# Kernel tuning notes

Measured on AMD Instinct MI355X. Metric: run time of the kernel, lower is better.

## Reference

```python
import jax, jax.numpy as jnp
import numpy as np

B, DIM, HGT, WID = 2, 384, 256, 256
HEADS = 8


def setup_inputs() -> dict:
    key = jax.random.key(0)
    k0, k1, k2, k3 = jax.random.split(key, 4)
    x = jax.random.normal(k0, (B, DIM, HGT, WID), jnp.float32)
    # 1x1 conv weights stored as (out_ch, in_ch); depthwise 3x3 as (out_ch, 1, 3, 3)
    qkv_w = jax.random.normal(k1, (3 * DIM, DIM), jnp.float32) * 0.02
    dw_w = jax.random.normal(k2, (3 * DIM, 1, 3, 3), jnp.float32) * 0.02
    proj_w = jax.random.normal(k3, (DIM, DIM), jnp.float32) * 0.02
    log_temp = jnp.zeros((HEADS, 1, 1), jnp.float32)  # nn.Parameter init zeros
    return {"x": x, "qkv_w": qkv_w, "dw_w": dw_w, "proj_w": proj_w, "log_temp": log_temp}


def _l2norm_lastdim(t):
    # F.normalize(t, dim=-1): t / max(||t||_2, eps), eps=1e-12
    n = jnp.linalg.norm(t, axis=-1, keepdims=True)
    return t / jnp.maximum(n, 1e-12)


def reference(x, qkv_w, dw_w, proj_w, log_temp):
    b, c, h, w = x.shape
    heads = log_temp.shape[0]
    head_dim = c // heads

    # 1x1 conv (pointwise) -> channel GEMM
    qkv = jnp.einsum('bchw,oc->bohw', x, qkv_w)
    # depthwise 3x3, stride 1, pad 1, groups = 3*dim
    qkv = jax.lax.conv_general_dilated(
        qkv, dw_w, window_strides=(1, 1), padding=[(1, 1), (1, 1)],
        dimension_numbers=('NCHW', 'OIHW', 'NCHW'), feature_group_count=3 * c)

    q, k, v = jnp.split(qkv, 3, axis=1)
    rs = lambda t: t.reshape(b, heads, head_dim, h * w)
    q, k, v = rs(q), rs(k), rs(v)

    q = _l2norm_lastdim(q)
    k = _l2norm_lastdim(k)

    # channel-wise attention: (head_dim x head_dim) logits per (b, head)
    attn = jnp.einsum('bhcn,bhdn->bhcd', q, k)
    attn = attn * (jax.nn.softplus(log_temp) + 1e-6)
    attn = jax.nn.softmax(attn, axis=-1)

    out = jnp.einsum('bhcd,bhdn->bhcn', attn, v).reshape(b, c, h, w)
    return jnp.einsum('bchw,oc->bohw', out, proj_w)
```

## Files before the change

kernel.cpp:

```cpp
#include <hip/hip_runtime.h>
#include <cstdint>
#include <cstddef>

#define HW 65536
#define HGT 256
#define WID 256
#define CDIM 384
#define C3 1152
#define HEADS 8
#define HD 48
#define NCHUNK 128
#define CHUNK (HW / NCHUNK)

typedef unsigned short u16;
typedef __attribute__((ext_vector_type(8))) short short8;
typedef __attribute__((ext_vector_type(16))) float f32x16;
typedef __attribute__((ext_vector_type(4))) u16 us4;

__device__ __forceinline__ u16 f2bf_rn(float f) {
  uint32_t u = __float_as_uint(f);
  return (u16)((u + 0x7FFFu + ((u >> 16) & 1u)) >> 16);
}
__device__ __forceinline__ float bf2f(u16 s) {
  return __uint_as_float((uint32_t)s << 16);
}

__device__ __forceinline__ void stage16(const void* g, void* lds_wave_base) {
  __builtin_amdgcn_global_load_lds(
      (const __attribute__((address_space(1))) void*)g,
      (__attribute__((address_space(3))) void*)lds_wave_base, 16, 0, 0);
}

__global__ __launch_bounds__(256)
void mfma_gemm_split(const u16* __restrict__ Ah, const u16* __restrict__ Al,
                     const u16* __restrict__ Bh, const u16* __restrict__ Bl,
                     float* __restrict__ C, int N, int K, int m_tiles) {
  __shared__ u16 sm[4][4096];
  const int t = threadIdx.x;
  const int wid = t >> 6, lane = t & 63;
  const int w = blockIdx.x;
  const int xcd = w & 7;
  const int slot = w >> 3;
  const int npx = (int)(gridDim.x >> 3) / m_tiles;
  const int m0 = (slot % m_tiles) * 128;
  const int n0 = (xcd * npx + slot / m_tiles) * 128;
  const int wm = (wid >> 1) * 64, wn = (wid & 1) * 64;

  f32x16 acc[2][2];
#pragma unroll
  for (int i = 0; i < 2; i++)
#pragma unroll
    for (int j = 0; j < 2; j++)
#pragma unroll
      for (int r = 0; r < 16; r++) acc[i][j][r] = 0.f;

  for (int k0 = 0; k0 < K; k0 += 32) {
#pragma unroll
    for (int u = 0; u < 2; u++) {
      const int s = u * 256 + wid * 64 + lane;
      const int row = s >> 2;
      const int cd = (s & 3) ^ ((row >> 1) & 3);
      const size_t offA = (size_t)(m0 + row) * K + k0 + cd * 8;
      const size_t offB = (size_t)(n0 + row) * K + k0 + cd * 8;
      const int lb = (u * 256 + wid * 64) * 8;
      stage16(Ah + offA, &sm[0][lb]);
      stage16(Al + offA, &sm[1][lb]);
      stage16(Bh + offB, &sm[2][lb]);
      stage16(Bl + offB, &sm[3][lb]);
    }
    __syncthreads();

    short8 ah[2][2], al[2][2], bh[2][2], bl[2][2];
#pragma unroll
    for (int f = 0; f < 2; f++)
#pragma unroll
      for (int ks = 0; ks < 2; ks++) {
        const int ra = wm + f * 32 + (lane & 31);
        const int ca = (ks * 2 + (lane >> 5)) ^ ((ra >> 1) & 3);
        const int oa = ra * 32 + ca * 8;
        ah[f][ks] = *(const short8*)&sm[0][oa];
        al[f][ks] = *(const short8*)&sm[1][oa];
        const int rb = wn + f * 32 + (lane & 31);
        const int cb = (ks * 2 + (lane >> 5)) ^ ((rb >> 1) & 3);
        const int ob = rb * 32 + cb * 8;
        bh[f][ks] = *(const short8*)&sm[2][ob];
        bl[f][ks] = *(const short8*)&sm[3][ob];
      }
#pragma unroll
    for (int ks = 0; ks < 2; ks++)
#pragma unroll
      for (int i = 0; i < 2; i++)
#pragma unroll
        for (int j = 0; j < 2; j++) {
          acc[i][j] = __builtin_amdgcn_mfma_f32_32x32x16_bf16(ah[i][ks], bh[j][ks], acc[i][j], 0, 0, 0);
          acc[i][j] = __builtin_amdgcn_mfma_f32_32x32x16_bf16(ah[i][ks], bl[j][ks], acc[i][j], 0, 0, 0);
          acc[i][j] = __builtin_amdgcn_mfma_f32_32x32x16_bf16(al[i][ks], bh[j][ks], acc[i][j], 0, 0, 0);
        }
    __syncthreads();
  }
  float* Cb = C + (size_t)(m0 + wm) * N + n0 + wn;
#pragma unroll
  for (int i = 0; i < 2; i++)
#pragma unroll
    for (int j = 0; j < 2; j++) {
      const int cc = j * 32 + (lane & 31);
#pragma unroll
      for (int reg = 0; reg < 16; reg++) {
        const int rr = i * 32 + (reg & 3) + 8 * (reg >> 2) + 4 * (lane >> 5);
        Cb[(size_t)rr * N + cc] = acc[i][j][reg];
      }
    }
}

__global__ __launch_bounds__(256)
void transpose_cvt(const float* __restrict__ in, u16* __restrict__ hi,
                   u16* __restrict__ lo) {
  __shared__ float tbuf[64][65];
  const int n0 = blockIdx.x * 64, c0 = blockIdx.y * 64;
  const int tx = threadIdx.x & 63, ty = threadIdx.x >> 6;
#pragma unroll
  for (int c = ty; c < 64; c += 4)
    tbuf[tx][c] = in[(size_t)(c0 + c) * HW + n0 + tx];
  __syncthreads();
  const int cq = (threadIdx.x & 15) << 2;
  const int nb = threadIdx.x >> 4;
#pragma unroll
  for (int p = 0; p < 4; p++) {
    const int n = p * 16 + nb;
    us4 h, l;
#pragma unroll
    for (int i = 0; i < 4; i++) {
      float f = tbuf[n][cq + i];
      u16 hb = f2bf_rn(f);
      h[i] = hb;
      l[i] = f2bf_rn(f - bf2f(hb));
    }
    *(us4*)&hi[(size_t)(n0 + n) * CDIM + c0 + cq] = h;
    *(us4*)&lo[(size_t)(n0 + n) * CDIM + c0 + cq] = l;
  }
}

__global__ __launch_bounds__(256)
void split_cvt(const float* __restrict__ in, u16* __restrict__ hi,
               u16* __restrict__ lo, int n) {
  int i = blockIdx.x * 256 + threadIdx.x;
  if (i < n) {
    float f = in[i];
    u16 hb = f2bf_rn(f);
    hi[i] = hb;
    lo[i] = f2bf_rn(f - bf2f(hb));
  }
}

__global__ __launch_bounds__(256)
void dwconv3x3(const float* __restrict__ in, const float* __restrict__ wgt,
               float* __restrict__ out) {
  const int ch = blockIdx.y;
  const int y0 = blockIdx.x * 4;
  const int t = threadIdx.x;
  __shared__ float rows[6][264];
  const float* inc = in + (size_t)ch * HW;
  float w9[9];
#pragma unroll
  for (int k = 0; k < 9; k++) w9[k] = wgt[ch * 9 + k];
  if (t < 6) {
    rows[t][0] = 0.f;
    rows[t][WID + 1] = 0.f;
  }
  for (int i = t; i < 6 * WID; i += 256) {
    int r = i >> 8;
    int x = i & 255;
    int y = y0 - 1 + r;
    rows[r][1 + x] = (y >= 0 && y < HGT) ? inc[(size_t)y * WID + x] : 0.f;
  }
  __syncthreads();
  const int x = t;
#pragma unroll
  for (int r = 0; r < 4; r++) {
    float s = 0.f;
#pragma unroll
    for (int ky = 0; ky < 3; ky++)
#pragma unroll
      for (int kx = 0; kx < 3; kx++)
        s = fmaf(w9[ky * 3 + kx], rows[r + ky][x + kx], s);
    out[(size_t)ch * HW + (size_t)(y0 + r) * WID + x] = s;
  }
}

__global__ __launch_bounds__(256)
void gram48(const float* __restrict__ qkvdw, float* __restrict__ Spart,
            float* __restrict__ qpart, float* __restrict__ kpart) {
  const int ck = blockIdx.x;
  const int h = blockIdx.y;
  const int t = threadIdx.x;
  const int ty = t >> 4, tx = t & 15;
  __shared__ float Qs[HD][33], Ks[HD][33];
  const float* qb = qkvdw + (size_t)(h * HD) * HW + ck * CHUNK;
  const float* kb = qkvdw + (size_t)(CDIM + h * HD) * HW + ck * CHUNK;
  float acc[3][3] = {{0, 0, 0}, {0, 0, 0}, {0, 0, 0}};
  float nacc = 0.f;
  for (int n0 = 0; n0 < CHUNK; n0 += 32) {
    __syncthreads();
    for (int i = t; i < HD * 32; i += 256) {
      int r = i >> 5, c = i & 31;
      Qs[r][c] = qb[(size_t)r * HW + n0 + c];
      Ks[r][c] = kb[(size_t)r * HW + n0 + c];
    }
    __syncthreads();
#pragma unroll 4
    for (int col = 0; col < 32; col++) {
      float qv[3], kv[3];
#pragma unroll
      for (int i = 0; i < 3; i++) qv[i] = Qs[ty * 3 + i][col];
#pragma unroll
      for (int j = 0; j < 3; j++) kv[j] = Ks[tx * 3 + j][col];
#pragma unroll
      for (int i = 0; i < 3; i++)
#pragma unroll
        for (int j = 0; j < 3; j++) acc[i][j] = fmaf(qv[i], kv[j], acc[i][j]);
    }
    if (t < HD) {
#pragma unroll 4
      for (int col = 0; col < 32; col++) nacc = fmaf(Qs[t][col], Qs[t][col], nacc);
    } else if (t >= 64 && t < 64 + HD) {
      int r = t - 64;
#pragma unroll 4
      for (int col = 0; col < 32; col++) nacc = fmaf(Ks[r][col], Ks[r][col], nacc);
    }
  }
  float* Sp = Spart + ((size_t)ck * HEADS + h) * HD * HD;
#pragma unroll
  for (int i = 0; i < 3; i++)
#pragma unroll
    for (int j = 0; j < 3; j++)
      Sp[(ty * 3 + i) * HD + tx * 3 + j] = acc[i][j];
  if (t < HD)
    qpart[((size_t)ck * HEADS + h) * HD + t] = nacc;
  else if (t >= 64 && t < 64 + HD)
    kpart[((size_t)ck * HEADS + h) * HD + (t - 64)] = nacc;
}

__global__ __launch_bounds__(64)
void attn_softmax(const float* __restrict__ Spart, const float* __restrict__ qpart,
                  const float* __restrict__ kpart, const float* __restrict__ log_temp,
                  float* __restrict__ attn) {
  const int h = blockIdx.x;
  const int c = threadIdx.x;
  __shared__ float kns[HD];
  const int cc = (c < HD) ? c : 0;
  float qs = 0.f, ks = 0.f;
  for (int ck = 0; ck < NCHUNK; ck++) {
    qs += qpart[((size_t)ck * HEADS + h) * HD + cc];
    ks += kpart[((size_t)ck * HEADS + h) * HD + cc];
  }
  float qn = fmaxf(sqrtf(qs), 1e-12f);
  if (c < HD) kns[c] = fmaxf(sqrtf(ks), 1e-12f);
  __syncthreads();
  if (c >= HD) return;
  float lt = log_temp[h];
  float temp = (lt > 20.f ? lt : log1pf(expf(lt))) + 1e-6f;
  float lg[HD];
#pragma unroll
  for (int d = 0; d < HD; d++) lg[d] = 0.f;
  for (int ck = 0; ck < NCHUNK; ck++) {
    const float* Sp = Spart + (((size_t)ck * HEADS + h) * HD + c) * HD;
#pragma unroll
    for (int d = 0; d < HD; d++) lg[d] += Sp[d];
  }
  float mx = -1e30f;
#pragma unroll
  for (int d = 0; d < HD; d++) {
    lg[d] = lg[d] / (qn * kns[d]) * temp;
    mx = fmaxf(mx, lg[d]);
  }
  float sum = 0.f;
#pragma unroll
  for (int d = 0; d < HD; d++) {
    lg[d] = expf(lg[d] - mx);
    sum += lg[d];
  }
  float inv = 1.f / sum;
#pragma unroll
  for (int d = 0; d < HD; d++) attn[((size_t)h * HD + c) * HD + d] = lg[d] * inv;
}

__global__ __launch_bounds__(256)
void fuse_proj(const float* __restrict__ proj_w, const float* __restrict__ attn,
               float* __restrict__ Mmat) {
  int idx = blockIdx.x * 256 + threadIdx.x;
  int o = idx / CDIM, j = idx % CDIM;
  int h = j / HD, d = j % HD;
  float s = 0.f;
#pragma unroll 8
  for (int c = 0; c < HD; c++)
    s = fmaf(proj_w[(size_t)o * CDIM + h * HD + c],
             attn[((size_t)h * HD + c) * HD + d], s);
  Mmat[idx] = s;
}

extern "C" void kernel_launch(void* const* d_in, const int* in_sizes, int n_in,
                              void* d_out, int out_size, void* d_ws, size_t ws_size,
                              hipStream_t stream) {
  const float* x = (const float*)d_in[0];
  const float* qkv_w = (const float*)d_in[1];
  const float* dw_w = (const float*)d_in[2];
  const float* proj_w = (const float*)d_in[3];
  const float* log_t = (const float*)d_in[4];
  float* out = (float*)d_out;

  float* ws = (float*)d_ws;
  const size_t C3HW = (size_t)C3 * HW;
  float* qkv = ws;
  float* qkvdw = qkv + C3HW;
  float* Spart = qkvdw + C3HW;
  float* qpart = Spart + (size_t)NCHUNK * HEADS * HD * HD;
  float* kpart = qpart + (size_t)NCHUNK * HEADS * HD;
  float* attn = kpart + (size_t)NCHUNK * HEADS * HD;
  float* Mmat = attn + (size_t)HEADS * HD * HD;
  u16* qkvw_h = (u16*)(Mmat + (size_t)CDIM * CDIM);
  u16* qkvw_l = qkvw_h + (size_t)C3 * CDIM;
  u16* Mh = (u16*)Spart;
  u16* Ml = Mh + (size_t)CDIM * CDIM;
  u16* xT_h = (u16*)qkvdw;
  u16* xT_l = xT_h + (size_t)HW * CDIM;
  u16* vT_h = (u16*)qkv;
  u16* vT_l = vT_h + (size_t)HW * CDIM;

  split_cvt<<<dim3((C3 * CDIM + 255) / 256), 256, 0, stream>>>(qkv_w, qkvw_h, qkvw_l,
                                                               C3 * CDIM);
  for (int b = 0; b < 2; b++) {
    const float* xb = x + (size_t)b * CDIM * HW;
    float* outb = out + (size_t)b * CDIM * HW;
    transpose_cvt<<<dim3(HW / 64, CDIM / 64), 256, 0, stream>>>(xb, xT_h, xT_l);
    mfma_gemm_split<<<dim3((C3 / 128) * (HW / 128)), 256, 0, stream>>>(
        qkvw_h, qkvw_l, xT_h, xT_l, qkv, HW, CDIM, C3 / 128);
    dwconv3x3<<<dim3(HGT / 4, C3), 256, 0, stream>>>(qkv, dw_w, qkvdw);
    gram48<<<dim3(NCHUNK, HEADS), 256, 0, stream>>>(qkvdw, Spart, qpart, kpart);
    attn_softmax<<<dim3(HEADS), 64, 0, stream>>>(Spart, qpart, kpart, log_t, attn);
    fuse_proj<<<dim3(CDIM * CDIM / 256), 256, 0, stream>>>(proj_w, attn, Mmat);
    split_cvt<<<dim3(CDIM * CDIM / 256), 256, 0, stream>>>(Mmat, Mh, Ml, CDIM * CDIM);
    transpose_cvt<<<dim3(HW / 64, CDIM / 64), 256, 0, stream>>>(
        qkvdw + (size_t)2 * CDIM * HW, vT_h, vT_l);
    mfma_gemm_split<<<dim3((CDIM / 128) * (HW / 128)), 256, 0, stream>>>(
        Mh, Ml, vT_h, vT_l, outb, HW, CDIM, CDIM / 128);
  }
}
```

Before: 1.763 ms.

## Fuse B-operand transpose and bf16 split into GEMM, reading fp32 directly

Measured after the change: 1.714 ms. -2.8%, faster.

```diff
diff --git a/kernel.cpp b/kernel.cpp
--- a/kernel.cpp
+++ b/kernel.cpp
@@ -32,10 +32,11 @@
 }
 
 __global__ __launch_bounds__(256)
-void mfma_gemm_split(const u16* __restrict__ Ah, const u16* __restrict__ Al,
-                     const u16* __restrict__ Bh, const u16* __restrict__ Bl,
-                     float* __restrict__ C, int N, int K, int m_tiles) {
-  __shared__ u16 sm[4][4096];
+void mfma_gemm_f32b(const u16* __restrict__ Ah, const u16* __restrict__ Al,
+                    const float* __restrict__ B, float* __restrict__ C,
+                    int N, int K, int m_tiles) {
+  __shared__ u16 smA[2][4096];
+  __shared__ float smB[4096];
   const int t = threadIdx.x;
   const int wid = t >> 6, lane = t & 63;
   const int w = blockIdx.x;
@@ -61,16 +62,22 @@
       const int row = s >> 2;
       const int cd = (s & 3) ^ ((row >> 1) & 3);
       const size_t offA = (size_t)(m0 + row) * K + k0 + cd * 8;
-      const size_t offB = (size_t)(n0 + row) * K + k0 + cd * 8;
       const int lb = (u * 256 + wid * 64) * 8;
-      stage16(Ah + offA, &sm[0][lb]);
-      stage16(Al + offA, &sm[1][lb]);
-      stage16(Bh + offB, &sm[2][lb]);
-      stage16(Bl + offB, &sm[3][lb]);
+      stage16(Ah + offA, &smA[0][lb]);
+      stage16(Al + offA, &smA[1][lb]);
+    }
+#pragma unroll
+    for (int u = 0; u < 4; u++) {
+      const int s = u * 256 + wid * 64 + lane;
+      const int row = s >> 5;
+      const int c5 = s & 31;
+      const size_t offB = (size_t)(k0 + row) * (size_t)N + n0 + c5 * 4;
+      const int lb = (u * 256 + wid * 64) * 4;
+      stage16(B + offB, &smB[lb]);
     }
     __syncthreads();
 
-    short8 ah[2][2], al[2][2], bh[2][2], bl[2][2];
+    short8 ah[2][2], al[2][2];
 #pragma unroll
     for (int f = 0; f < 2; f++)
 #pragma unroll
@@ -78,13 +85,25 @@
         const int ra = wm + f * 32 + (lane & 31);
         const int ca = (ks * 2 + (lane >> 5)) ^ ((ra >> 1) & 3);
         const int oa = ra * 32 + ca * 8;
-        ah[f][ks] = *(const short8*)&sm[0][oa];
-        al[f][ks] = *(const short8*)&sm[1][oa];
-        const int rb = wn + f * 32 + (lane & 31);
-        const int cb = (ks * 2 + (lane >> 5)) ^ ((rb >> 1) & 3);
-        const int ob = rb * 32 + cb * 8;
-        bh[f][ks] = *(const short8*)&sm[2][ob];
-        bl[f][ks] = *(const short8*)&sm[3][ob];
+        ah[f][ks] = *(const short8*)&smA[0][oa];
+        al[f][ks] = *(const short8*)&smA[1][oa];
+      }
+    short8 bh[2][2], bl[2][2];
+#pragma unroll
+    for (int f = 0; f < 2; f++)
+#pragma unroll
+      for (int ks = 0; ks < 2; ks++) {
+        const int ncol = wn + f * 32 + (lane & 31);
+        const int kb = ks * 16 + (lane >> 5) * 8;
+#pragma unroll
+        for (int e = 0; e < 8; e++) {
+          const float v = smB[(kb + e) * 128 + ncol];
+          const uint32_t uv = __float_as_uint(v);
+          const u16 h = (u16)(uv >> 16);
+          const u16 l = f2bf_rn(v - bf2f(h));
+          bh[f][ks][e] = (short)h;
+          bl[f][ks][e] = (short)l;
+        }
       }
 #pragma unroll
     for (int ks = 0; ks < 2; ks++)
@@ -110,34 +129,6 @@
         Cb[(size_t)rr * N + cc] = acc[i][j][reg];
       }
     }
-}
-
-__global__ __launch_bounds__(256)
-void transpose_cvt(const float* __restrict__ in, u16* __restrict__ hi,
-                   u16* __restrict__ lo) {
-  __shared__ float tbuf[64][65];
-  const int n0 = blockIdx.x * 64, c0 = blockIdx.y * 64;
-  const int tx = threadIdx.x & 63, ty = threadIdx.x >> 6;
-#pragma unroll
-  for (int c = ty; c < 64; c += 4)
-    tbuf[tx][c] = in[(size_t)(c0 + c) * HW + n0 + tx];
-  __syncthreads();
-  const int cq = (threadIdx.x & 15) << 2;
-  const int nb = threadIdx.x >> 4;
-#pragma unroll
-  for (int p = 0; p < 4; p++) {
-    const int n = p * 16 + nb;
-    us4 h, l;
-#pragma unroll
-    for (int i = 0; i < 4; i++) {
-      float f = tbuf[n][cq + i];
-      u16 hb = f2bf_rn(f);
-      h[i] = hb;
-      l[i] = f2bf_rn(f - bf2f(hb));
-    }
-    *(us4*)&hi[(size_t)(n0 + n) * CDIM + c0 + cq] = h;
-    *(us4*)&lo[(size_t)(n0 + n) * CDIM + c0 + cq] = l;
-  }
 }
 
 __global__ __launch_bounds__(256)
@@ -319,29 +310,22 @@
   float* Mmat = attn + (size_t)HEADS * HD * HD;
   u16* qkvw_h = (u16*)(Mmat + (size_t)CDIM * CDIM);
   u16* qkvw_l = qkvw_h + (size_t)C3 * CDIM;
-  u16* Mh = (u16*)Spart;
+  u16* Mh = qkvw_l + (size_t)C3 * CDIM;
   u16* Ml = Mh + (size_t)CDIM * CDIM;
-  u16* xT_h = (u16*)qkvdw;
-  u16* xT_l = xT_h + (size_t)HW * CDIM;
-  u16* vT_h = (u16*)qkv;
-  u16* vT_l = vT_h + (size_t)HW * CDIM;
 
   split_cvt<<<dim3((C3 * CDIM + 255) / 256), 256, 0, stream>>>(qkv_w, qkvw_h, qkvw_l,
                                                                C3 * CDIM);
   for (int b = 0; b < 2; b++) {
     const float* xb = x + (size_t)b * CDIM * HW;
     float* outb = out + (size_t)b * CDIM * HW;
-    transpose_cvt<<<dim3(HW / 64, CDIM / 64), 256, 0, stream>>>(xb, xT_h, xT_l);
-    mfma_gemm_split<<<dim3((C3 / 128) * (HW / 128)), 256, 0, stream>>>(
-        qkvw_h, qkvw_l, xT_h, xT_l, qkv, HW, CDIM, C3 / 128);
+    mfma_gemm_f32b<<<dim3((C3 / 128) * (HW / 128)), 256, 0, stream>>>(
+        qkvw_h, qkvw_l, xb, qkv, HW, CDIM, C3 / 128);
     dwconv3x3<<<dim3(HGT / 4, C3), 256, 0, stream>>>(qkv, dw_w, qkvdw);
     gram48<<<dim3(NCHUNK, HEADS), 256, 0, stream>>>(qkvdw, Spart, qpart, kpart);
     attn_softmax<<<dim3(HEADS), 64, 0, stream>>>(Spart, qpart, kpart, log_t, attn);
     fuse_proj<<<dim3(CDIM * CDIM / 256), 256, 0, stream>>>(proj_w, attn, Mmat);
     split_cvt<<<dim3(CDIM * CDIM / 256), 256, 0, stream>>>(Mmat, Mh, Ml, CDIM * CDIM);
-    transpose_cvt<<<dim3(HW / 64, CDIM / 64), 256, 0, stream>>>(
-        qkvdw + (size_t)2 * CDIM * HW, vT_h, vT_l);
-    mfma_gemm_split<<<dim3((CDIM / 128) * (HW / 128)), 256, 0, stream>>>(
-        Mh, Ml, vT_h, vT_l, outb, HW, CDIM, CDIM / 128);
-  }
-}
+    mfma_gemm_f32b<<<dim3((CDIM / 128) * (HW / 128)), 256, 0, stream>>>(
+        Mh, Ml, qkvdw + (size_t)2 * CDIM * HW, outb, HW, CDIM, CDIM / 128);
+  }
+}
```
